# Performance work log

Hardware: AMD Instinct MI355X
Metric: run time of the kernel (lower is better)

Reference implementation:

```python
import jax, jax.numpy as jnp
import numpy as np
import math

N_FILT = 512
FILT_DIM = 1025
BATCH = 64
FS = 16000.0
FFT_N = 512  # hard-coded n=512 in the original np.fft.rfft call


def setup_inputs() -> dict:
    key = jax.random.key(0)
    kq, = jax.random.split(key, 1)
    # Q factors: positive, realistic filter quality factors in [2, 10)
    Q = jax.random.uniform(kq, (BATCH, N_FILT), dtype=jnp.float32) * 8.0 + 2.0
    # center frequencies exactly as the module computes f_cos:
    # fdelta = fs/2/N_filt; fc = arange(fdelta/2, fs/2, fdelta)
    fdelta = FS / 2.0 / N_FILT
    fc = jnp.asarray(np.arange(fdelta / 2.0, FS / 2.0, fdelta), dtype=jnp.float32)
    return {"Q": Q, "fc": fc}


def reference(Q, fc):
    # Q: [B, F] quality factors, fc: [F] center frequencies (Hz)
    T = FILT_DIM - 1
    # nT = t_right * fs = [1, 2, ..., N-1]
    n = jnp.arange(1, T + 1, dtype=Q.dtype)                      # [T]
    BW = fc[None, :] / Q                                         # [B, F]
    alpha = BW * (0.5 * math.sqrt(2.0 * math.pi))                # [B, F]
    b = alpha / FS                                               # [B, F]
    omega_c = (2.0 * math.pi / FS) * fc                          # [F]
    # y[b,f,t] = exp(-(b*n)^2) * cos(omega_c * n)
    env = jnp.exp(-jnp.square(b[:, :, None] * n))                # [B, F, T]
    carrier = jnp.cos(omega_c[None, :, None] * n)                # [1, F, T] bcast
    y = env * carrier                                            # [B, F, T]
    # per-filter max |rfft| over batch and frequency bins (detached in original)
    fft_mag = jnp.abs(jnp.fft.rfft(y, n=FFT_N, axis=-1))         # [B, F, 257]
    maxfft = jax.lax.stop_gradient(jnp.max(fft_mag, axis=(0, 2)))  # [F]
    filters = jnp.flip(y / maxfft[None, :, None], axis=-1)       # [B, F, T]
    return filters
```

## Files before the change

### kernel.cpp

```cpp
#include <hip/hip_runtime.h>


#define BCOEF_K 7.8332133582218756e-05f
#define INV_FS  6.25e-05f
#define TWO_PI  6.28318530717958647692f
#define PI_F    3.14159265358979323846f

typedef float vf4 __attribute__((ext_vector_type(4)));

__device__ __forceinline__ float fast_carrier(float fcn, float n) {
  float rev = fcn * n;
  float fr  = rev - floorf(rev);
  return __cosf(TWO_PI * fr);
}

__device__ __forceinline__ float fast_env(float x) { return __expf(-x * x); }

__global__ __launch_bounds__(256) void k_maxfft(const float* __restrict__ Q,
                                                const float* __restrict__ fc,
                                                float* __restrict__ ws) {
  const int tid  = threadIdx.x;
  const int w    = tid >> 6;
  const int lane = tid & 63;
  const int sig  = blockIdx.x * 4 + w;
  const int f    = sig & 511;
  const int bb   = sig >> 9;

  __shared__ __align__(16) float ybuf[4][512];

  const float fcv = fc[f];
  const float q   = Q[bb * 512 + f];
  const float bc  = (fcv / q) * BCOEF_K;
  const float fcn = fcv * INV_FS;

  const float nstar = 4.0f / bc;
  const int   N_eff = (nstar >= 510.0f) ? 512 : ((int)nstar + 2);
  const int   jmax  = (N_eff + 3) >> 2;
  const int   n4    = jmax << 2;

  float* yw = &ybuf[w][0];
  const int nit_g = (n4 + 63) >> 6;
  for (int r = 0; r < nit_g; ++r) {
    const int idx = (r << 6) + lane;
    const float n = (float)(idx + 1);
    const float v = fast_env(bc * n) * fast_carrier(fcn, n);
    if (idx < n4) yw[idx] = v;
  }
  asm volatile("s_waitcnt lgkmcnt(0)" ::: "memory");

  const int kci = (int)(fcn * 512.0f + 0.5f);
  const int k   = min(max(kci - 31 + lane, 0), 256);
  const float c = 2.0f * cosf((float)k * (PI_F / 256.0f));

  float s1 = 0.0f, s2 = 0.0f;
  const float4* y4 = (const float4*)yw;
  #pragma unroll 4
  for (int j = 0; j < jmax; ++j) {
    const float4 x = y4[j];
    float s;
    s = fmaf(c, s1, x.x - s2); s2 = s1; s1 = s;
    s = fmaf(c, s1, x.y - s2); s2 = s1; s1 = s;
    s = fmaf(c, s1, x.z - s2); s2 = s1; s1 = s;
    s = fmaf(c, s1, x.w - s2); s2 = s1; s1 = s;
  }
  float mx = fmaf(s1, s1, fmaf(s2, s2, -(c * s1 * s2)));

  #pragma unroll
  for (int d = 32; d > 0; d >>= 1) mx = fmaxf(mx, __shfl_xor(mx, d));
  if (lane == 0) ws[f * 64 + bb] = mx;
}

__global__ __launch_bounds__(256) void k_write(const float* __restrict__ Q,
                                               const float* __restrict__ fc,
                                               const float* __restrict__ ws,
                                               float* __restrict__ out) {
  const int blk = blockIdx.x;
  const int f   = blk & 511;
  const int bb  = blk >> 9;
  const int tid = threadIdx.x;

  float mx = ws[f * 64 + (tid & 63)];
  #pragma unroll
  for (int d = 32; d > 0; d >>= 1) mx = fmaxf(mx, __shfl_xor(mx, d));

  const float fcv = fc[f];
  const float q   = Q[bb * 512 + f];
  const float bc  = (fcv / q) * BCOEF_K;
  const float fcn = fcv * INV_FS;
  const float nstar = 4.0f / bc;

  const int t0 = tid * 4;
  vf4 r = {0.0f, 0.0f, 0.0f, 0.0f};
  if ((float)(1021 - t0) <= nstar) {
    const float inv = rsqrtf(mx);
    const float n0 = (float)(1024 - t0);
    const float n1 = (float)(1023 - t0);
    const float n2 = (float)(1022 - t0);
    const float n3 = (float)(1021 - t0);
    r.x = fast_env(bc * n0) * fast_carrier(fcn, n0) * inv;
    r.y = fast_env(bc * n1) * fast_carrier(fcn, n1) * inv;
    r.z = fast_env(bc * n2) * fast_carrier(fcn, n2) * inv;
    r.w = fast_env(bc * n3) * fast_carrier(fcn, n3) * inv;
  }
  __builtin_nontemporal_store(r, &((vf4*)out)[blk * 256 + tid]);
}

extern "C" void kernel_launch(void* const* d_in, const int* in_sizes, int n_in,
                              void* d_out, int out_size, void* d_ws, size_t ws_size,
                              hipStream_t stream) {
  const float* Q  = (const float*)d_in[0];
  const float* fc = (const float*)d_in[1];
  float* out      = (float*)d_out;
  float* ws       = (float*)d_ws;

  k_maxfft<<<64 * 512 / 4, 256, 0, stream>>>(Q, fc, ws);
  k_write <<<64 * 512,     256, 0, stream>>>(Q, fc, ws, out);
}
```

Baseline: 164.7 us.

## Compute max-FFT via lane-parallel DFT over few bins with DPP wave sums

Replaces the per-lane Goertzel recurrence over 64 candidate bins (with a shared-memory signal buffer) with a register-resident signal and a direct DFT. Each lane accumulates its own samples against twiddles for a narrow window of bins around the carrier frequency, five bins per pass, and DPP wave reductions produce the sums. The window widens to all bins up to 256 only when a bandwidth test suggests the peak may lie far from the carrier. This removes the LDS traffic and the serial recurrence, but assumes the peak magnitude lies within a few bins of the carrier for narrow filters, and the twiddle recurrences may accumulate rounding error.

```diff
diff --git a/kernel.cpp b/kernel.cpp
--- a/kernel.cpp
+++ b/kernel.cpp
@@ -4,7 +4,6 @@
 #define BCOEF_K 7.8332133582218756e-05f
 #define INV_FS  6.25e-05f
 #define TWO_PI  6.28318530717958647692f
-#define PI_F    3.14159265358979323846f
 
 typedef float vf4 __attribute__((ext_vector_type(4)));
 
@@ -13,8 +12,21 @@
   float fr  = rev - floorf(rev);
   return __cosf(TWO_PI * fr);
 }
+__device__ __forceinline__ float fast_env(float x) { return __expf(-x * x); }
 
-__device__ __forceinline__ float fast_env(float x) { return __expf(-x * x); }
+#define DPP_STEP(x, ctrl, rmask)                                              \
+  x += __int_as_float(__builtin_amdgcn_update_dpp(                            \
+      0, __float_as_int(x), ctrl, rmask, 0xf, false))
+
+__device__ __forceinline__ float wave_sum(float x) {
+  DPP_STEP(x, 0x111, 0xf);
+  DPP_STEP(x, 0x112, 0xf);
+  DPP_STEP(x, 0x114, 0xf);
+  DPP_STEP(x, 0x118, 0xf);
+  DPP_STEP(x, 0x142, 0xa);
+  DPP_STEP(x, 0x143, 0xc);
+  return __int_as_float(__builtin_amdgcn_readlane(__float_as_int(x), 63));
+}
 
 __global__ __launch_bounds__(256) void k_maxfft(const float* __restrict__ Q,
                                                 const float* __restrict__ fc,
@@ -26,47 +38,80 @@
   const int f    = sig & 511;
   const int bb   = sig >> 9;
 
-  __shared__ __align__(16) float ybuf[4][512];
-
   const float fcv = fc[f];
   const float q   = Q[bb * 512 + f];
   const float bc  = (fcv / q) * BCOEF_K;
   const float fcn = fcv * INV_FS;
 
   const float nstar = 4.0f / bc;
-  const int   N_eff = (nstar >= 510.0f) ? 512 : ((int)nstar + 2);
-  const int   jmax  = (N_eff + 3) >> 2;
-  const int   n4    = jmax << 2;
+  const int   R = (nstar >= 505.0f) ? 8 : (((int)nstar + 2 + 63) >> 6);
 
-  float* yw = &ybuf[w][0];
-  const int nit_g = (n4 + 63) >> 6;
-  for (int r = 0; r < nit_g; ++r) {
-    const int idx = (r << 6) + lane;
-    const float n = (float)(idx + 1);
-    const float v = fast_env(bc * n) * fast_carrier(fcn, n);
-    if (idx < n4) yw[idx] = v;
+  const float n0 = (float)(lane + 1);
+  float yv[8];
+  #pragma unroll
+  for (int r = 0; r < 8; ++r) {
+    if (r < R) {
+      const float n = n0 + (float)(r << 6);
+      yv[r] = fast_env(bc * n) * fast_carrier(fcn, n);
+    }
   }
-  asm volatile("s_waitcnt lgkmcnt(0)" ::: "memory");
 
   const int kci = (int)(fcn * 512.0f + 0.5f);
-  const int k   = min(max(kci - 31 + lane, 0), 256);
-  const float c = 2.0f * cosf((float)k * (PI_F / 256.0f));
+  const int lo  = kci - 2;
+  int       hi  = kci + 2;
+  if (407.0f * bc > (float)(512 - 2 * kci)) hi = 256;
 
-  float s1 = 0.0f, s2 = 0.0f;
-  const float4* y4 = (const float4*)yw;
-  #pragma unroll 4
-  for (int j = 0; j < jmax; ++j) {
-    const float4 x = y4[j];
-    float s;
-    s = fmaf(c, s1, x.x - s2); s2 = s1; s1 = s;
-    s = fmaf(c, s1, x.y - s2); s2 = s1; s1 = s;
-    s = fmaf(c, s1, x.z - s2); s2 = s1; s1 = s;
-    s = fmaf(c, s1, x.w - s2); s2 = s1; s1 = s;
+  float mx = 0.0f;
+  for (int c = lo; c <= hi; c += 5) {
+    const float lrev = n0 * (1.0f / 512.0f);
+    const float revc = (float)c * lrev;
+    const float ac   = TWO_PI * (revc - floorf(revc));
+    const float ad   = TWO_PI * lrev;
+    const float dre  = __cosf(ad), dim = -__sinf(ad);
+    float pre[5], pim[5];
+    pre[0] = __cosf(ac); pim[0] = -__sinf(ac);
+    #pragma unroll
+    for (int j = 1; j < 5; ++j) {
+      pre[j] = pre[j-1] * dre - pim[j-1] * dim;
+      pim[j] = pre[j-1] * dim + pim[j-1] * dre;
+    }
+    float er[5], ei[5];
+    {
+      const float rev8 = (float)c * 0.125f;
+      const float ae   = TWO_PI * (rev8 - floorf(rev8));
+      er[0] = __cosf(ae); ei[0] = -__sinf(ae);
+      const float hr = 0.70710678118654752440f;
+      #pragma unroll
+      for (int j = 1; j < 5; ++j) {
+        er[j] = (er[j-1] + ei[j-1]) * hr;
+        ei[j] = (ei[j-1] - er[j-1]) * hr;
+      }
+    }
+
+    float Xre[5] = {0,0,0,0,0}, Xim[5] = {0,0,0,0,0};
+    #pragma unroll
+    for (int r = 0; r < 8; ++r) {
+      if (r < R) {
+        const float y = yv[r];
+        #pragma unroll
+        for (int j = 0; j < 5; ++j) {
+          Xre[j] = fmaf(y, pre[j], Xre[j]);
+          Xim[j] = fmaf(y, pim[j], Xim[j]);
+          const float t = pre[j] * er[j] - pim[j] * ei[j];
+          pim[j] = fmaf(pre[j], ei[j], pim[j] * er[j]);
+          pre[j] = t;
+        }
+      }
+    }
+
+    #pragma unroll
+    for (int j = 0; j < 5; ++j) {
+      const float re = wave_sum(Xre[j]);
+      const float im = wave_sum(Xim[j]);
+      mx = fmaxf(mx, fmaf(re, re, im * im));
+    }
   }
-  float mx = fmaf(s1, s1, fmaf(s2, s2, -(c * s1 * s2)));
 
-  #pragma unroll
-  for (int d = 32; d > 0; d >>= 1) mx = fmaxf(mx, __shfl_xor(mx, d));
   if (lane == 0) ws[f * 64 + bb] = mx;
 }
 
```

Measured after the change: 172.1 us. 1.04x slower.

## Replace per-lane Goertzel with chunked direct DFT over bin groups plus reduction kernel

Applied to the files above, without the earlier changes.

Replaces the Goertzel-per-lane max-FFT computation with a direct DFT that splits the signal into 64-sample chunks and 8-bin groups. Work items are spread across 8 blocks per filter, with one lane per batch element, and partial sums go to workspace. A new reduce kernel sums the partials and takes the max magnitude. The bin range near the carrier is widened when the envelope is broad. This adds a kernel launch and workspace traffic, and it recomputes the signal per bin group. The aim is better parallelism and accuracy over a wider bin coverage.

```diff
diff --git a/kernel.cpp b/kernel.cpp
--- a/kernel.cpp
+++ b/kernel.cpp
@@ -4,7 +4,14 @@
 #define BCOEF_K 7.8332133582218756e-05f
 #define INV_FS  6.25e-05f
 #define TWO_PI  6.28318530717958647692f
-#define PI_F    3.14159265358979323846f
+
+#define NF 512
+#define NB 64
+#define GROUP 8
+#define MAXIT 16
+#define ITEM_STRIDE (GROUP * NB * 2)
+#define F_STRIDE    (MAXIT * ITEM_STRIDE)
+#define B_OFFSET    (NF * F_STRIDE)
 
 typedef float vf4 __attribute__((ext_vector_type(4)));
 
@@ -13,61 +20,115 @@
   float fr  = rev - floorf(rev);
   return __cosf(TWO_PI * fr);
 }
-
 __device__ __forceinline__ float fast_env(float x) { return __expf(-x * x); }
 
-__global__ __launch_bounds__(256) void k_maxfft(const float* __restrict__ Q,
-                                                const float* __restrict__ fc,
-                                                float* __restrict__ ws) {
-  const int tid  = threadIdx.x;
-  const int w    = tid >> 6;
-  const int lane = tid & 63;
-  const int sig  = blockIdx.x * 4 + w;
-  const int f    = sig & 511;
-  const int bb   = sig >> 9;
+__device__ __forceinline__ void f_geometry(float fcv, float bc_lane,
+                                           int& nchunk, int& ngroups, int& kb) {
+  float nsf = 4.0f / bc_lane;
+  #pragma unroll
+  for (int d = 32; d > 0; d >>= 1) nsf = fmaxf(nsf, __shfl_xor(nsf, d));
+  const int nsamp = min(512, (int)nsf + 2);
+  nchunk = (nsamp + 63) >> 6;
 
-  __shared__ __align__(16) float ybuf[4][512];
+  const float fcn = fcv * INV_FS;
+  const int kci = (int)(fcn * 512.0f + 0.5f);
+  kb = kci - 3;
+  const float bcw = fcv * (BCOEF_K * 0.5f);
+  ngroups = 1;
+  if (407.0f * bcw > (float)(512 - 2 * kci))
+    ngroups = ((256 - kb) >> 3) + 1;
+  if (nchunk * ngroups > MAXIT) ngroups = MAXIT / nchunk;
+}
+
+__global__ __launch_bounds__(64) void k_dft(const float* __restrict__ Q,
+                                            const float* __restrict__ fc,
+                                            float* __restrict__ ws) {
+  const int s    = blockIdx.x & 7;
+  const int f    = blockIdx.x >> 3;
+  const int lane = threadIdx.x;
 
   const float fcv = fc[f];
-  const float q   = Q[bb * 512 + f];
+  const float q   = Q[lane * NF + f];
   const float bc  = (fcv / q) * BCOEF_K;
   const float fcn = fcv * INV_FS;
 
-  const float nstar = 4.0f / bc;
-  const int   N_eff = (nstar >= 510.0f) ? 512 : ((int)nstar + 2);
-  const int   jmax  = (N_eff + 3) >> 2;
-  const int   n4    = jmax << 2;
+  int nchunk, ngroups, kb;
+  f_geometry(fcv, bc, nchunk, ngroups, kb);
+  const int nitems = nchunk * ngroups;
 
-  float* yw = &ybuf[w][0];
-  const int nit_g = (n4 + 63) >> 6;
-  for (int r = 0; r < nit_g; ++r) {
-    const int idx = (r << 6) + lane;
-    const float n = (float)(idx + 1);
-    const float v = fast_env(bc * n) * fast_carrier(fcn, n);
-    if (idx < n4) yw[idx] = v;
+  for (int it = s; it < nitems; it += 8) {
+    const int c  = it % nchunk;
+    const int g  = it / nchunk;
+    const int k0 = kb + (g << 3);
+    const int n0 = (c << 6) + 1;
+
+    float pre[GROUP], pim[GROUP], dre[GROUP], dim[GROUP];
+    #pragma unroll
+    for (int j = 0; j < GROUP; ++j) {
+      const float kj = (float)(k0 + j);
+      float rp = kj * (float)n0 * (1.0f / 512.0f);
+      rp -= floorf(rp);
+      pre[j] = __cosf(TWO_PI * rp);
+      pim[j] = -__sinf(TWO_PI * rp);
+      float rd = kj * (1.0f / 512.0f);
+      rd -= floorf(rd);
+      dre[j] = __cosf(TWO_PI * rd);
+      dim[j] = -__sinf(TWO_PI * rd);
+    }
+
+    float Xre[GROUP], Xim[GROUP];
+    #pragma unroll
+    for (int j = 0; j < GROUP; ++j) { Xre[j] = 0.0f; Xim[j] = 0.0f; }
+
+    for (int i = 0; i < 64; ++i) {
+      const float nf = (float)(n0 + i);
+      const float y  = fast_env(bc * nf) * fast_carrier(fcn, nf);
+      #pragma unroll
+      for (int j = 0; j < GROUP; ++j) {
+        Xre[j] = fmaf(y, pre[j], Xre[j]);
+        Xim[j] = fmaf(y, pim[j], Xim[j]);
+        const float t = pre[j] * dre[j] - pim[j] * dim[j];
+        pim[j] = fmaf(pre[j], dim[j], pim[j] * dre[j]);
+        pre[j] = t;
+      }
+    }
+
+    float* base = ws + (size_t)(f * MAXIT + it) * ITEM_STRIDE + lane * 2;
+    #pragma unroll
+    for (int j = 0; j < GROUP; ++j) {
+      base[j * NB * 2]     = Xre[j];
+      base[j * NB * 2 + 1] = Xim[j];
+    }
   }
-  asm volatile("s_waitcnt lgkmcnt(0)" ::: "memory");
+}
 
-  const int kci = (int)(fcn * 512.0f + 0.5f);
-  const int k   = min(max(kci - 31 + lane, 0), 256);
-  const float c = 2.0f * cosf((float)k * (PI_F / 256.0f));
+__global__ __launch_bounds__(64) void k_reduce(const float* __restrict__ Q,
+                                               const float* __restrict__ fc,
+                                               float* __restrict__ ws) {
+  const int f    = blockIdx.x;
+  const int lane = threadIdx.x;
 
-  float s1 = 0.0f, s2 = 0.0f;
-  const float4* y4 = (const float4*)yw;
-  #pragma unroll 4
-  for (int j = 0; j < jmax; ++j) {
-    const float4 x = y4[j];
-    float s;
-    s = fmaf(c, s1, x.x - s2); s2 = s1; s1 = s;
-    s = fmaf(c, s1, x.y - s2); s2 = s1; s1 = s;
-    s = fmaf(c, s1, x.z - s2); s2 = s1; s1 = s;
-    s = fmaf(c, s1, x.w - s2); s2 = s1; s1 = s;
+  const float fcv = fc[f];
+  const float q   = Q[lane * NF + f];
+  const float bc  = (fcv / q) * BCOEF_K;
+
+  int nchunk, ngroups, kb;
+  f_geometry(fcv, bc, nchunk, ngroups, kb);
+
+  float mx = 0.0f;
+  for (int g = 0; g < ngroups; ++g) {
+    for (int j = 0; j < GROUP; ++j) {
+      float re = 0.0f, im = 0.0f;
+      for (int c = 0; c < nchunk; ++c) {
+        const float* p = ws + (size_t)(f * MAXIT + g * nchunk + c) * ITEM_STRIDE
+                         + j * NB * 2 + lane * 2;
+        re += p[0];
+        im += p[1];
+      }
+      mx = fmaxf(mx, fmaf(re, re, im * im));
+    }
   }
-  float mx = fmaf(s1, s1, fmaf(s2, s2, -(c * s1 * s2)));
-
-  #pragma unroll
-  for (int d = 32; d > 0; d >>= 1) mx = fmaxf(mx, __shfl_xor(mx, d));
-  if (lane == 0) ws[f * 64 + bb] = mx;
+  ws[B_OFFSET + f * NB + lane] = mx;
 }
 
 __global__ __launch_bounds__(256) void k_write(const float* __restrict__ Q,
@@ -79,12 +140,12 @@
   const int bb  = blk >> 9;
   const int tid = threadIdx.x;
 
-  float mx = ws[f * 64 + (tid & 63)];
+  float mx = ws[B_OFFSET + f * NB + (tid & 63)];
   #pragma unroll
   for (int d = 32; d > 0; d >>= 1) mx = fmaxf(mx, __shfl_xor(mx, d));
 
   const float fcv = fc[f];
-  const float q   = Q[bb * 512 + f];
+  const float q   = Q[bb * NF + f];
   const float bc  = (fcv / q) * BCOEF_K;
   const float fcn = fcv * INV_FS;
   const float nstar = 4.0f / bc;
@@ -113,6 +174,7 @@
   float* out      = (float*)d_out;
   float* ws       = (float*)d_ws;
 
-  k_maxfft<<<64 * 512 / 4, 256, 0, stream>>>(Q, fc, ws);
-  k_write <<<64 * 512,     256, 0, stream>>>(Q, fc, ws, out);
+  k_dft   <<<NF * 8,  64,  0, stream>>>(Q, fc, ws);
+  k_reduce<<<NF,      64,  0, stream>>>(Q, fc, ws);
+  k_write <<<64 * NF, 256, 0, stream>>>(Q, fc, ws, out);
 }
```

New measurement: 211.4 us. +28.3%, slower.
